# Kernel optimization log

Hardware: AMD Instinct MI355X
Metric: run time of the kernel (lower is better)

## Reference

```python
import jax, jax.numpy as jnp
import numpy as np

D_MODEL = 1024
NUM_HEADS = 16
HEAD_DIM = D_MODEL // NUM_HEADS
B, S = 4, 2048
NEG = -1e10


def setup_inputs() -> dict:
    key = jax.random.key(0)
    ks = jax.random.split(key, 10)
    s = 1.0 / np.sqrt(D_MODEL)
    x = jax.random.normal(ks[0], (B, S, D_MODEL), dtype=jnp.float32)
    mask = jnp.ones((B, S, S), dtype=jnp.int32)
    Wq = jax.random.uniform(ks[1], (D_MODEL, D_MODEL), jnp.float32, -s, s)
    bq = jnp.zeros((D_MODEL,), jnp.float32)
    Wk = jax.random.uniform(ks[2], (D_MODEL, D_MODEL), jnp.float32, -s, s)
    bk = jnp.zeros((D_MODEL,), jnp.float32)
    Wv = jax.random.uniform(ks[3], (D_MODEL, D_MODEL), jnp.float32, -s, s)
    bv = jnp.zeros((D_MODEL,), jnp.float32)
    Wo = jax.random.uniform(ks[4], (D_MODEL, D_MODEL), jnp.float32, -s, s)
    bo = jnp.zeros((D_MODEL,), jnp.float32)
    return {"x": x, "mask": mask, "Wq": Wq, "bq": bq, "Wk": Wk, "bk": bk,
            "Wv": Wv, "bv": bv, "Wo": Wo, "bo": bo}


def reference(x, mask, Wq, bq, Wk, bk, Wv, bv, Wo, bo):
    # x: [B,S,D]; projections then split into heads -> [B,H,S,hd]
    def split_heads(t):
        return t.reshape(B, S, NUM_HEADS, HEAD_DIM).transpose(0, 2, 1, 3)

    q = split_heads(x @ Wq + bq)
    k = split_heads(x @ Wk + bk)
    v = split_heads(x @ Wv + bv)
    scale = jnp.sqrt(jnp.float32(HEAD_DIM))
    # energy: [B,H,S,S]
    energy = jnp.einsum('bhqd,bhkd->bhqk', q, k) / scale
    energy = jnp.where(mask[:, None, :, :] == 0, jnp.float32(NEG), energy)
    attn = jax.nn.softmax(energy, axis=-1)
    # dropout is identity in eval mode
    out = jnp.einsum('bhqk,bhkd->bhqd', attn, v)
    out = out.transpose(0, 2, 1, 3).reshape(B, S, D_MODEL)
    return out @ Wo + bo
```

## Files before the change

### kernel.cpp

```cpp
#include <hip/hip_runtime.h>
#include <stdint.h>


#define SS 2048
#define NH 16

typedef __bf16 bf16x8 __attribute__((ext_vector_type(8)));
typedef float f32x4 __attribute__((ext_vector_type(4)));

__device__ __forceinline__ unsigned short f2bf(float f) {
  union { float f; unsigned int u; } v; v.f = f;
  unsigned int u = v.u;
  return (unsigned short)((u + 0x7fffu + ((u >> 16) & 1u)) >> 16);
}

__device__ __forceinline__ unsigned int cvtpk(float a, float b) {
  unsigned int r;
  asm("v_cvt_pk_bf16_f32 %0, %1, %2" : "=v"(r) : "v"(a), "v"(b));
  return r;
}

__device__ __forceinline__ float ex2(float x) {
  float r; asm("v_exp_f32 %0, %1" : "=v"(r) : "v"(x)); return r;
}

__device__ __forceinline__ void swap32(unsigned int& a, unsigned int& b) {
  asm volatile("v_permlane32_swap_b32 %0, %1" : "+v"(a), "+v"(b));
}
__device__ __forceinline__ void swap16(unsigned int& a, unsigned int& b) {
  asm volatile("v_permlane16_swap_b32 %0, %1" : "+v"(a), "+v"(b));
}

__device__ __forceinline__ void gload_lds16(const void* g, void* l) {
  __builtin_amdgcn_global_load_lds(
      (__attribute__((address_space(1))) void*)(void*)g,
      (__attribute__((address_space(3))) void*)l,
      16, 0, 0);
}

__global__ __launch_bounds__(256) void k_prep(const float* __restrict__ x,
                                              const float* __restrict__ W0,
                                              const float* __restrict__ W1,
                                              const float* __restrict__ W2,
                                              const float* __restrict__ W3,
                                              const int* __restrict__ mask,
                                              unsigned short* __restrict__ xb,
                                              unsigned short* __restrict__ Wt,
                                              int* __restrict__ flg) {
  __shared__ float t[64][65];
  __shared__ int s4[4];
  const int bid = blockIdx.x;
  const int tid = threadIdx.x;

  if (bid < 8192) {
    long i = ((long)bid * 256 + tid) * 4;
    float4 v = *(const float4*)(x + i);
    uint2 o;
    o.x = cvtpk(v.x, v.y);
    o.y = cvtpk(v.z, v.w);
    *(uint2*)(xb + i) = o;
  } else if (bid < 9216) {
    int inner = bid - 8192;
    int bx = inner & 15, by = (inner >> 4) & 15, bz = inner >> 8;
    const float* W = bz == 0 ? W0 : bz == 1 ? W1 : bz == 2 ? W2 : W3;
    unsigned short* dst = Wt + (size_t)bz * 1024 * 1024;
    int r0 = by * 64, c0 = bx * 64;
    int tr = tid >> 6, tc = tid & 63;
#pragma unroll
    for (int i = 0; i < 16; i++) {
      int r = tr + i * 4;
      t[r][tc] = W[(size_t)(r0 + r) * 1024 + c0 + tc];
    }
    __syncthreads();
#pragma unroll
    for (int i = 0; i < 16; i++) {
      int r = tr + i * 4;
      dst[(size_t)(c0 + r) * 1024 + r0 + tc] = f2bf(t[tc][r]);
    }
  } else {
    int inner = bid - 9216;
    int kt = inner & 31, qb = (inner >> 5) & 15, b = inner >> 9;
    const int* M = mask + ((size_t)b * SS + qb * 128) * SS + kt * 64;
    int ok = 1;
#pragma unroll
    for (int i = 0; i < 8; i++) {
      int r = (tid >> 4) + i * 16;
      int4 v = *(const int4*)(M + (size_t)r * SS + (tid & 15) * 4);
      ok &= (v.x != 0) & (v.y != 0) & (v.z != 0) & (v.w != 0);
    }
    ok = __all(ok) ? 1 : 0;
    if ((tid & 63) == 0) s4[tid >> 6] = ok;
    __syncthreads();
    if (tid == 0) flg[((size_t)b * 16 + qb) * 32 + kt] = s4[0] & s4[1] & s4[2] & s4[3];
  }
}

__global__ __launch_bounds__(256) void k_gemmQKV(const unsigned short* __restrict__ A,
                                                 const unsigned short* __restrict__ Wt,
                                                 const float* __restrict__ bq,
                                                 const float* __restrict__ bk,
                                                 const float* __restrict__ bv,
                                                 unsigned short* __restrict__ Qb,
                                                 unsigned short* __restrict__ Kb,
                                                 unsigned short* __restrict__ Vtp) {
  constexpr int K = 1024, N = 1024;
  __shared__ unsigned short lA[128 * 64];
  __shared__ unsigned short lB[128 * 64];
  const int tid = threadIdx.x;
  const int lane = tid & 63, wave = tid >> 6;
  const int wr = wave >> 1, wc = wave & 1;
  const int g = lane >> 4, c = lane & 15;

  const int mat = blockIdx.x >> 9;
  const int inner = blockIdx.x & 511;
  const int xcd = inner & 7, idx = inner >> 3;
  const int by = xcd * 8 + (idx >> 3), bx = idx & 7;
  const long brow = (long)by * 128, bcol = (long)bx * 128;

  const unsigned short* Bt = Wt + ((size_t)mat << 20);
  const float* bias = mat == 0 ? bq : (mat == 1 ? bk : bv);

  f32x4 acc[4][4] = {};

  int sr[4], sch[4];
#pragma unroll
  for (int j = 0; j < 4; j++) {
    int p = j * 4096 + tid * 16;
    int r = p >> 7;
    int sl = (p >> 4) & 7;
    sr[j] = r;
    sch[j] = (sl ^ (r & 7)) * 8;
  }
  char* lbaseA = (char*)lA + wave * 1024;
  char* lbaseB = (char*)lB + wave * 1024;

  for (int k0 = 0; k0 < K; k0 += 64) {
#pragma unroll
    for (int j = 0; j < 4; j++) {
      gload_lds16(A + (brow + sr[j]) * K + k0 + sch[j], lbaseA + j * 4096);
      gload_lds16(Bt + (bcol + sr[j]) * K + k0 + sch[j], lbaseB + j * 4096);
    }
    __syncthreads();
#pragma unroll
    for (int ks = 0; ks < 2; ks++) {
      bf16x8 af[4], bfr[4];
#pragma unroll
      for (int m = 0; m < 4; m++) {
        int ra = wr * 64 + m * 16 + c;
        af[m] = *(const bf16x8*)((const char*)lA + ra * 128 + ((ks * 64 + g * 16) ^ ((ra & 7) << 4)));
        int rb = wc * 64 + m * 16 + c;
        bfr[m] = *(const bf16x8*)((const char*)lB + rb * 128 + ((ks * 64 + g * 16) ^ ((rb & 7) << 4)));
      }
      __builtin_amdgcn_s_setprio(1);
#pragma unroll
      for (int m = 0; m < 4; m++)
#pragma unroll
        for (int n = 0; n < 4; n++)
          acc[m][n] = __builtin_amdgcn_mfma_f32_16x16x32_bf16(af[m], bfr[n], acc[m][n], 0, 0, 0);
      __builtin_amdgcn_s_setprio(0);
    }
    __syncthreads();
  }

  const float scale = (mat == 0) ? 0.180336880111120f  : 1.0f;
#pragma unroll
  for (int m = 0; m < 4; m++) {
#pragma unroll
    for (int n = 0; n < 4; n++) {
      long row0 = brow + wr * 64 + m * 16 + g * 4;
      long col = bcol + wc * 64 + n * 16 + c;
      float bv_ = bias[col];
      if (mat == 2) {
        long b_ = row0 >> 11, s = row0 & 2047;
        size_t base = ((size_t)(b_ * NH + (col >> 6)) * 64 + (col & 63)) * SS + s;
        ushort4 pk;
        pk.x = f2bf(acc[m][n][0] + bv_);
        pk.y = f2bf(acc[m][n][1] + bv_);
        pk.z = f2bf(acc[m][n][2] + bv_);
        pk.w = f2bf(acc[m][n][3] + bv_);
        *(ushort4*)(Vtp + base) = pk;
      } else {
        unsigned short* C = mat ? Kb : Qb;
#pragma unroll
        for (int r = 0; r < 4; r++)
          C[(row0 + r) * N + col] = f2bf((acc[m][n][r] + bv_) * scale);
      }
    }
  }
}

__global__ __launch_bounds__(256) void k_gemmO(const unsigned short* __restrict__ A,
                                               const unsigned short* __restrict__ Bt,
                                               const float* __restrict__ bias,
                                               float* __restrict__ Cout) {
  constexpr int K = 1024, N = 1024;
  __shared__ unsigned short lA[128 * 64];
  __shared__ unsigned short lB[128 * 64];
  const int tid = threadIdx.x;
  const int lane = tid & 63, wave = tid >> 6;
  const int wr = wave >> 1, wc = wave & 1;
  const int g = lane >> 4, c = lane & 15;

  const int bid = blockIdx.x;
  const int xcd = bid & 7, idx = bid >> 3;
  const int by = xcd * 8 + (idx >> 3), bx = idx & 7;
  const long brow = (long)by * 128, bcol = (long)bx * 128;

  f32x4 acc[4][4] = {};

  int sr[4], sch[4];
#pragma unroll
  for (int j = 0; j < 4; j++) {
    int p = j * 4096 + tid * 16;
    int r = p >> 7;
    int sl = (p >> 4) & 7;
    sr[j] = r;
    sch[j] = (sl ^ (r & 7)) * 8;
  }
  char* lbaseA = (char*)lA + wave * 1024;
  char* lbaseB = (char*)lB + wave * 1024;

  for (int k0 = 0; k0 < K; k0 += 64) {
#pragma unroll
    for (int j = 0; j < 4; j++) {
      gload_lds16(A + (brow + sr[j]) * K + k0 + sch[j], lbaseA + j * 4096);
      gload_lds16(Bt + (bcol + sr[j]) * K + k0 + sch[j], lbaseB + j * 4096);
    }
    __syncthreads();
#pragma unroll
    for (int ks = 0; ks < 2; ks++) {
      bf16x8 af[4], bfr[4];
#pragma unroll
      for (int m = 0; m < 4; m++) {
        int ra = wr * 64 + m * 16 + c;
        af[m] = *(const bf16x8*)((const char*)lA + ra * 128 + ((ks * 64 + g * 16) ^ ((ra & 7) << 4)));
        int rb = wc * 64 + m * 16 + c;
        bfr[m] = *(const bf16x8*)((const char*)lB + rb * 128 + ((ks * 64 + g * 16) ^ ((rb & 7) << 4)));
      }
      __builtin_amdgcn_s_setprio(1);
#pragma unroll
      for (int m = 0; m < 4; m++)
#pragma unroll
        for (int n = 0; n < 4; n++)
          acc[m][n] = __builtin_amdgcn_mfma_f32_16x16x32_bf16(af[m], bfr[n], acc[m][n], 0, 0, 0);
      __builtin_amdgcn_s_setprio(0);
    }
    __syncthreads();
  }

#pragma unroll
  for (int m = 0; m < 4; m++) {
#pragma unroll
    for (int n = 0; n < 4; n++) {
      long row0 = brow + wr * 64 + m * 16 + g * 4;
      long col = bcol + wc * 64 + n * 16 + c;
      float bv = bias[col];
#pragma unroll
      for (int r = 0; r < 4; r++)
        Cout[(row0 + r) * N + col] = acc[m][n][r] + bv;
    }
  }
}

__global__ __launch_bounds__(256, 4) void k_flash(const unsigned short* __restrict__ Q,
                                                  const unsigned short* __restrict__ Kb,
                                                  const unsigned short* __restrict__ Vt,
                                                  const int* __restrict__ mask,
                                                  const int* __restrict__ flg,
                                                  unsigned short* __restrict__ O) {
  __shared__ unsigned short lK[3][4096];
  __shared__ unsigned short lV[2][4096];
  const int tid = threadIdx.x, lane = tid & 63, w = tid >> 6;
  const int g = lane >> 4, c = lane & 15;

  const int bid = blockIdx.x;
  const int xcd = bid & 7, jj = bid >> 3;
  const int qb = jj & 15, Ghi = jj >> 4;
  const int G = xcd * 8 + Ghi;
  const int h = G & 15, b = G >> 4;

  const int q0 = qb * 128 + w * 32;
  const long mrow0 = (long)b * SS + q0;

  const unsigned short* Kbase = Kb + (size_t)b * SS * 1024 + h * 64;
  const unsigned short* Vbase = Vt + (size_t)((b * NH + h) * 64) * SS;
  const int* Mbase = mask + ((size_t)b * SS + q0) * SS;
  const int* Fbase = flg + ((size_t)b * 16 + qb) * 32;

  int allok = 1;
#pragma unroll
  for (int i = 0; i < 32; i++) allok &= Fbase[i];
  allok = __builtin_amdgcn_readfirstlane(allok);

  bf16x8 qf[2][2];
#pragma unroll
  for (int rt = 0; rt < 2; rt++)
#pragma unroll
    for (int ks = 0; ks < 2; ks++)
      qf[rt][ks] = *(const bf16x8*)(Q + (mrow0 + rt * 16 + c) * 1024 + h * 64 + ks * 32 + g * 8);

  const int pB = tid * 16;
  const int r0 = pB >> 7;
  const int co = (((pB >> 4) & 7) ^ (r0 & 7)) * 8;
  const unsigned short* gK = Kbase + (size_t)r0 * 1024 + co;
  const unsigned short* gV = Vbase + (size_t)r0 * SS + co;
  const int wb = w * 1024;

  char* sk0 = (char*)&lK[0][0];
  char* sk1 = (char*)&lK[1][0];
  char* sk2 = (char*)&lK[2][0];
  char* sv0 = (char*)&lV[0][0];
  char* sv1 = (char*)&lV[1][0];

#define STAGE_K(kt_, dst_) do { \
    const unsigned short* aK_ = gK + (size_t)(kt_) * (64 * 1024); \
    gload_lds16(aK_, (dst_) + wb); \
    gload_lds16(aK_ + 32 * 1024, (dst_) + wb + 4096); } while (0)
#define STAGE_V(kt_, dst_) do { \
    const unsigned short* aV_ = gV + (size_t)(kt_) * 64; \
    gload_lds16(aV_, (dst_) + wb); \
    gload_lds16(aV_ + 32 * (size_t)SS, (dst_) + wb + 4096); } while (0)

  STAGE_K(0, sk0);
  STAGE_V(0, sv0);
  STAGE_K(1, sk1);

  float mst[2] = {8.0f, 8.0f}, lst[2] = {0.0f, 0.0f};
  f32x4 o[2][4] = {};

  for (int kt = 0; kt < SS / 64; kt++) {
    if (kt < SS / 64 - 1) asm volatile("s_waitcnt vmcnt(2)" ::: "memory");
    else                  asm volatile("s_waitcnt vmcnt(0)" ::: "memory");
    __builtin_amdgcn_s_barrier();
    __builtin_amdgcn_sched_barrier(0);
    if (kt + 1 < SS / 64) STAGE_V(kt + 1, sv1);
    if (kt + 2 < SS / 64) STAGE_K(kt + 2, sk2);

    bf16x8 kf[4][2];
#pragma unroll
    for (int ct = 0; ct < 4; ct++)
#pragma unroll
      for (int ks = 0; ks < 2; ks++)
        kf[ct][ks] = *(const bf16x8*)(sk0 + (ct * 16 + c) * 128 +
                                      ((ks * 64 + g * 16) ^ ((c & 7) << 4)));

    f32x4 sc[2][4];
#pragma unroll
    for (int rt = 0; rt < 2; rt++)
#pragma unroll
      for (int ct = 0; ct < 4; ct++)
#pragma unroll
        for (int r = 0; r < 4; r++) sc[rt][ct][r] = -mst[rt];
    __builtin_amdgcn_s_setprio(1);
#pragma unroll
    for (int ks = 0; ks < 2; ks++)
#pragma unroll
      for (int rt = 0; rt < 2; rt++)
#pragma unroll
        for (int ct = 0; ct < 4; ct++)
          sc[rt][ct] = __builtin_amdgcn_mfma_f32_16x16x32_bf16(kf[ct][ks], qf[rt][ks], sc[rt][ct], 0, 0, 0);
    __builtin_amdgcn_s_setprio(0);

    if (!allok) {
      const int key0 = kt * 64;
#pragma unroll
      for (int rt = 0; rt < 2; rt++)
#pragma unroll
        for (int ct = 0; ct < 4; ct++)
#pragma unroll
          for (int r = 0; r < 4; r++) {
            int mv = Mbase[(size_t)(rt * 16 + c) * SS + key0 + ct * 16 + g * 4 + r];
            if (mv == 0) sc[rt][ct][r] = -1e10f;
          }
    }

    float pm[2];
#pragma unroll
    for (int rt = 0; rt < 2; rt++) {
      f32x4 m4;
#pragma unroll
      for (int r = 0; r < 4; r++)
        m4[r] = fmaxf(fmaxf(sc[rt][0][r], sc[rt][1][r]), fmaxf(sc[rt][2][r], sc[rt][3][r]));
      pm[rt] = fmaxf(fmaxf(m4[0], m4[1]), fmaxf(m4[2], m4[3]));
    }
    if (__any((pm[0] > 8.0f) | (pm[1] > 8.0f))) {
#pragma unroll
      for (int rt = 0; rt < 2; rt++) {
        float tmv = pm[rt];
        tmv = fmaxf(tmv, __shfl_xor(tmv, 16, 64));
        tmv = fmaxf(tmv, __shfl_xor(tmv, 32, 64));
        float dpos = fmaxf(tmv, 0.0f);
        float sf = ex2(-dpos);
        mst[rt] += dpos;
        lst[rt] *= sf;
#pragma unroll
        for (int ct = 0; ct < 4; ct++)
#pragma unroll
          for (int r = 0; r < 4; r++) { o[rt][ct][r] *= sf; sc[rt][ct][r] -= dpos; }
      }
    }

    union PU { unsigned int wd[4]; bf16x8 v; };
    PU pf[2][2];
#pragma unroll
    for (int rt = 0; rt < 2; rt++) {
      f32x4 ts4 = {0.0f, 0.0f, 0.0f, 0.0f};
      unsigned int Wd[4][2];
#pragma unroll
      for (int ct = 0; ct < 4; ct++) {
        f32x4 p;
#pragma unroll
        for (int r = 0; r < 4; r++) {
          p[r] = ex2(sc[rt][ct][r]);
          ts4[r] += p[r];
        }
        Wd[ct][0] = cvtpk(p[0], p[1]);
        Wd[ct][1] = cvtpk(p[2], p[3]);
      }
#pragma unroll
      for (int ks = 0; ks < 2; ks++)
#pragma unroll
        for (int hh = 0; hh < 2; hh++) {
          unsigned int a = Wd[2 * ks][hh], bb = Wd[2 * ks + 1][hh];
          swap32(a, bb);
          swap16(a, bb);
          pf[rt][ks].wd[hh] = a;
          pf[rt][ks].wd[2 + hh] = bb;
        }
      lst[rt] += (ts4[0] + ts4[1]) + (ts4[2] + ts4[3]);
    }

    bf16x8 vf[4][2];
#pragma unroll
    for (int ct = 0; ct < 4; ct++)
#pragma unroll
      for (int ks = 0; ks < 2; ks++)
        vf[ct][ks] = *(const bf16x8*)(sv0 + (ct * 16 + c) * 128 +
                                      ((ks * 64 + g * 16) ^ ((c & 7) << 4)));
    __builtin_amdgcn_s_setprio(1);
#pragma unroll
    for (int rt = 0; rt < 2; rt++)
#pragma unroll
      for (int ct = 0; ct < 4; ct++)
#pragma unroll
        for (int ks = 0; ks < 2; ks++)
          o[rt][ct] = __builtin_amdgcn_mfma_f32_16x16x32_bf16(vf[ct][ks], pf[rt][ks].v, o[rt][ct], 0, 0, 0);
    __builtin_amdgcn_s_setprio(0);

    char* tk = sk0; sk0 = sk1; sk1 = sk2; sk2 = tk;
    char* tv = sv0; sv0 = sv1; sv1 = tv;
  }

#pragma unroll
  for (int rt = 0; rt < 2; rt++) {
    float t = lst[rt];
    t += __shfl_xor(t, 16, 64);
    t += __shfl_xor(t, 32, 64);
    float inv = 1.0f / t;
#pragma unroll
    for (int ct = 0; ct < 4; ct++) {
      uint2 pk;
      pk.x = cvtpk(o[rt][ct][0] * inv, o[rt][ct][1] * inv);
      pk.y = cvtpk(o[rt][ct][2] * inv, o[rt][ct][3] * inv);
      *(uint2*)(O + (mrow0 + rt * 16 + c) * 1024 + h * 64 + ct * 16 + g * 4) = pk;
    }
  }
#undef STAGE_K
#undef STAGE_V
}

extern "C" void kernel_launch(void* const* d_in, const int* in_sizes, int n_in,
                              void* d_out, int out_size, void* d_ws, size_t ws_size,
                              hipStream_t stream) {
  const float* x  = (const float*)d_in[0];
  const int* mask = (const int*)d_in[1];
  const float* Wq = (const float*)d_in[2];
  const float* bq = (const float*)d_in[3];
  const float* Wk = (const float*)d_in[4];
  const float* bk = (const float*)d_in[5];
  const float* Wv = (const float*)d_in[6];
  const float* bv = (const float*)d_in[7];
  const float* Wo = (const float*)d_in[8];
  const float* bo = (const float*)d_in[9];

  char* ws = (char*)d_ws;
  unsigned short* xb = (unsigned short*)ws;
  unsigned short* Wt = (unsigned short*)(ws + (16ull << 20));
  unsigned short* Qb = (unsigned short*)(ws + (24ull << 20));
  unsigned short* Kb = (unsigned short*)(ws + (40ull << 20));
  unsigned short* Vt = (unsigned short*)(ws + (56ull << 20));
  int* flg = (int*)d_out;

  k_prep<<<11264, 256, 0, stream>>>(x, Wq, Wk, Wv, Wo, mask, xb, Wt, flg);
  k_gemmQKV<<<1536, 256, 0, stream>>>(xb, Wt, bq, bk, bv, Qb, Kb, Vt);
  k_flash<<<1024, 256, 0, stream>>>(Qb, Kb, Vt, mask, flg, xb);
  k_gemmO<<<512, 256, 0, stream>>>(xb, Wt + (3u << 20), bo, (float*)d_out);
}
```

Baseline: 200.3 us.

## Halve flash-attention tiles to 16 query rows per wave and 32-key blocks

Shrinks the attention work per wave from 32 query rows to 16, and the key/value block from 64 to 32 keys. The grid doubles to 2048 blocks and LDS buffers are halved, with a new swizzle for the narrower V tile. The aim is more concurrent blocks and lower register and LDS pressure. In exchange, each staged K/V tile is reused by half as many query rows, so global and LDS traffic per FLOP doubles, and there are twice as many loop iterations and barriers.

```diff
diff --git a/kernel.cpp b/kernel.cpp
--- a/kernel.cpp
+++ b/kernel.cpp
@@ -268,43 +268,43 @@
                                                   const int* __restrict__ mask,
                                                   const int* __restrict__ flg,
                                                   unsigned short* __restrict__ O) {
-  __shared__ unsigned short lK[3][4096];
-  __shared__ unsigned short lV[2][4096];
+  __shared__ unsigned short lK[3][2048];
+  __shared__ unsigned short lV[2][2048];
   const int tid = threadIdx.x, lane = tid & 63, w = tid >> 6;
   const int g = lane >> 4, c = lane & 15;
 
   const int bid = blockIdx.x;
   const int xcd = bid & 7, jj = bid >> 3;
-  const int qb = jj & 15, Ghi = jj >> 4;
+  const int qb = jj & 31, Ghi = jj >> 5;
   const int G = xcd * 8 + Ghi;
   const int h = G & 15, b = G >> 4;
 
-  const int q0 = qb * 128 + w * 32;
+  const int q0 = qb * 64 + w * 16;
   const long mrow0 = (long)b * SS + q0;
 
   const unsigned short* Kbase = Kb + (size_t)b * SS * 1024 + h * 64;
   const unsigned short* Vbase = Vt + (size_t)((b * NH + h) * 64) * SS;
   const int* Mbase = mask + ((size_t)b * SS + q0) * SS;
-  const int* Fbase = flg + ((size_t)b * 16 + qb) * 32;
+  const int* Fbase = flg + ((size_t)b * 16 + (q0 >> 7)) * 32;
 
   int allok = 1;
 #pragma unroll
   for (int i = 0; i < 32; i++) allok &= Fbase[i];
   allok = __builtin_amdgcn_readfirstlane(allok);
 
-  bf16x8 qf[2][2];
-#pragma unroll
-  for (int rt = 0; rt < 2; rt++)
-#pragma unroll
-    for (int ks = 0; ks < 2; ks++)
-      qf[rt][ks] = *(const bf16x8*)(Q + (mrow0 + rt * 16 + c) * 1024 + h * 64 + ks * 32 + g * 8);
+  bf16x8 qf[2];
+#pragma unroll
+  for (int ks = 0; ks < 2; ks++)
+    qf[ks] = *(const bf16x8*)(Q + (mrow0 + c) * 1024 + h * 64 + ks * 32 + g * 8);
 
   const int pB = tid * 16;
-  const int r0 = pB >> 7;
-  const int co = (((pB >> 4) & 7) ^ (r0 & 7)) * 8;
-  const unsigned short* gK = Kbase + (size_t)r0 * 1024 + co;
-  const unsigned short* gV = Vbase + (size_t)r0 * SS + co;
-  const int wb = w * 1024;
+  const int rK = pB >> 7;
+  const int coK = ((((pB >> 4) & 7) ^ (rK & 7))) * 8;
+  const unsigned short* gK = Kbase + (size_t)rK * 1024 + coK;
+  const int rV = pB >> 6;
+  const int swV = (rV & 3) ^ ((rV >> 2) & 3);
+  const int coV = (((pB >> 4) & 3) ^ swV) * 8;
+  const unsigned short* gV = Vbase + (size_t)rV * SS + coV;
 
   char* sk0 = (char*)&lK[0][0];
   char* sk1 = (char*)&lK[1][0];
@@ -312,158 +312,133 @@
   char* sv0 = (char*)&lV[0][0];
   char* sv1 = (char*)&lV[1][0];
 
-#define STAGE_K(kt_, dst_) do { \
-    const unsigned short* aK_ = gK + (size_t)(kt_) * (64 * 1024); \
-    gload_lds16(aK_, (dst_) + wb); \
-    gload_lds16(aK_ + 32 * 1024, (dst_) + wb + 4096); } while (0)
-#define STAGE_V(kt_, dst_) do { \
-    const unsigned short* aV_ = gV + (size_t)(kt_) * 64; \
-    gload_lds16(aV_, (dst_) + wb); \
-    gload_lds16(aV_ + 32 * (size_t)SS, (dst_) + wb + 4096); } while (0)
+#define STAGE_K(kt_, dst_) gload_lds16(gK + (size_t)(kt_) * (32 * 1024), (dst_) + pB)
+#define STAGE_V(kt_, dst_) gload_lds16(gV + (size_t)(kt_) * 32, (dst_) + pB)
 
   STAGE_K(0, sk0);
   STAGE_V(0, sv0);
   STAGE_K(1, sk1);
 
-  float mst[2] = {8.0f, 8.0f}, lst[2] = {0.0f, 0.0f};
-  f32x4 o[2][4] = {};
-
-  for (int kt = 0; kt < SS / 64; kt++) {
-    if (kt < SS / 64 - 1) asm volatile("s_waitcnt vmcnt(2)" ::: "memory");
-    else                  asm volatile("s_waitcnt vmcnt(0)" ::: "memory");
+  float mst = 8.0f, lst = 0.0f;
+  f32x4 o[4] = {};
+
+  constexpr int NT = SS / 32;
+  for (int kt = 0; kt < NT; kt++) {
+    if (kt < NT - 1) asm volatile("s_waitcnt vmcnt(1)" ::: "memory");
+    else             asm volatile("s_waitcnt vmcnt(0)" ::: "memory");
     __builtin_amdgcn_s_barrier();
     __builtin_amdgcn_sched_barrier(0);
-    if (kt + 1 < SS / 64) STAGE_V(kt + 1, sv1);
-    if (kt + 2 < SS / 64) STAGE_K(kt + 2, sk2);
-
-    bf16x8 kf[4][2];
-#pragma unroll
-    for (int ct = 0; ct < 4; ct++)
+    if (kt + 1 < NT) STAGE_V(kt + 1, sv1);
+    if (kt + 2 < NT) STAGE_K(kt + 2, sk2);
+
+    bf16x8 kf[2][2];
+#pragma unroll
+    for (int ct = 0; ct < 2; ct++)
 #pragma unroll
       for (int ks = 0; ks < 2; ks++)
         kf[ct][ks] = *(const bf16x8*)(sk0 + (ct * 16 + c) * 128 +
                                       ((ks * 64 + g * 16) ^ ((c & 7) << 4)));
 
-    f32x4 sc[2][4];
-#pragma unroll
-    for (int rt = 0; rt < 2; rt++)
+    f32x4 sc[2];
+#pragma unroll
+    for (int ct = 0; ct < 2; ct++)
+#pragma unroll
+      for (int r = 0; r < 4; r++) sc[ct][r] = -mst;
+    __builtin_amdgcn_s_setprio(1);
+#pragma unroll
+    for (int ks = 0; ks < 2; ks++)
+#pragma unroll
+      for (int ct = 0; ct < 2; ct++)
+        sc[ct] = __builtin_amdgcn_mfma_f32_16x16x32_bf16(kf[ct][ks], qf[ks], sc[ct], 0, 0, 0);
+    __builtin_amdgcn_s_setprio(0);
+
+    if (!allok) {
+      const int key0 = kt * 32;
+#pragma unroll
+      for (int ct = 0; ct < 2; ct++)
+#pragma unroll
+        for (int r = 0; r < 4; r++) {
+          int mv = Mbase[(size_t)c * SS + key0 + ct * 16 + g * 4 + r];
+          if (mv == 0) sc[ct][r] = -1e10f;
+        }
+    }
+
+    f32x4 m4;
+#pragma unroll
+    for (int r = 0; r < 4; r++) m4[r] = fmaxf(sc[0][r], sc[1][r]);
+    float pm = fmaxf(fmaxf(m4[0], m4[1]), fmaxf(m4[2], m4[3]));
+    if (__any(pm > 8.0f)) {
+      float tmv = pm;
+      tmv = fmaxf(tmv, __shfl_xor(tmv, 16, 64));
+      tmv = fmaxf(tmv, __shfl_xor(tmv, 32, 64));
+      float dpos = fmaxf(tmv, 0.0f);
+      float sf = ex2(-dpos);
+      mst += dpos;
+      lst *= sf;
 #pragma unroll
       for (int ct = 0; ct < 4; ct++)
 #pragma unroll
-        for (int r = 0; r < 4; r++) sc[rt][ct][r] = -mst[rt];
-    __builtin_amdgcn_s_setprio(1);
-#pragma unroll
-    for (int ks = 0; ks < 2; ks++)
-#pragma unroll
-      for (int rt = 0; rt < 2; rt++)
-#pragma unroll
-        for (int ct = 0; ct < 4; ct++)
-          sc[rt][ct] = __builtin_amdgcn_mfma_f32_16x16x32_bf16(kf[ct][ks], qf[rt][ks], sc[rt][ct], 0, 0, 0);
-    __builtin_amdgcn_s_setprio(0);
-
-    if (!allok) {
-      const int key0 = kt * 64;
-#pragma unroll
-      for (int rt = 0; rt < 2; rt++)
-#pragma unroll
-        for (int ct = 0; ct < 4; ct++)
-#pragma unroll
-          for (int r = 0; r < 4; r++) {
-            int mv = Mbase[(size_t)(rt * 16 + c) * SS + key0 + ct * 16 + g * 4 + r];
-            if (mv == 0) sc[rt][ct][r] = -1e10f;
-          }
-    }
-
-    float pm[2];
-#pragma unroll
-    for (int rt = 0; rt < 2; rt++) {
-      f32x4 m4;
-#pragma unroll
-      for (int r = 0; r < 4; r++)
-        m4[r] = fmaxf(fmaxf(sc[rt][0][r], sc[rt][1][r]), fmaxf(sc[rt][2][r], sc[rt][3][r]));
-      pm[rt] = fmaxf(fmaxf(m4[0], m4[1]), fmaxf(m4[2], m4[3]));
-    }
-    if (__any((pm[0] > 8.0f) | (pm[1] > 8.0f))) {
-#pragma unroll
-      for (int rt = 0; rt < 2; rt++) {
-        float tmv = pm[rt];
-        tmv = fmaxf(tmv, __shfl_xor(tmv, 16, 64));
-        tmv = fmaxf(tmv, __shfl_xor(tmv, 32, 64));
-        float dpos = fmaxf(tmv, 0.0f);
-        float sf = ex2(-dpos);
-        mst[rt] += dpos;
-        lst[rt] *= sf;
-#pragma unroll
-        for (int ct = 0; ct < 4; ct++)
-#pragma unroll
-          for (int r = 0; r < 4; r++) { o[rt][ct][r] *= sf; sc[rt][ct][r] -= dpos; }
-      }
+        for (int r = 0; r < 4; r++) o[ct][r] *= sf;
+#pragma unroll
+      for (int ct = 0; ct < 2; ct++)
+#pragma unroll
+        for (int r = 0; r < 4; r++) sc[ct][r] -= dpos;
     }
 
     union PU { unsigned int wd[4]; bf16x8 v; };
-    PU pf[2][2];
-#pragma unroll
-    for (int rt = 0; rt < 2; rt++) {
+    PU pf;
+    {
       f32x4 ts4 = {0.0f, 0.0f, 0.0f, 0.0f};
-      unsigned int Wd[4][2];
-#pragma unroll
-      for (int ct = 0; ct < 4; ct++) {
+      unsigned int Wd[2][2];
+#pragma unroll
+      for (int ct = 0; ct < 2; ct++) {
         f32x4 p;
 #pragma unroll
         for (int r = 0; r < 4; r++) {
-          p[r] = ex2(sc[rt][ct][r]);
+          p[r] = ex2(sc[ct][r]);
           ts4[r] += p[r];
         }
         Wd[ct][0] = cvtpk(p[0], p[1]);
         Wd[ct][1] = cvtpk(p[2], p[3]);
       }
 #pragma unroll
-      for (int ks = 0; ks < 2; ks++)
-#pragma unroll
-        for (int hh = 0; hh < 2; hh++) {
-          unsigned int a = Wd[2 * ks][hh], bb = Wd[2 * ks + 1][hh];
-          swap32(a, bb);
-          swap16(a, bb);
-          pf[rt][ks].wd[hh] = a;
-          pf[rt][ks].wd[2 + hh] = bb;
-        }
-      lst[rt] += (ts4[0] + ts4[1]) + (ts4[2] + ts4[3]);
-    }
-
-    bf16x8 vf[4][2];
+      for (int hh = 0; hh < 2; hh++) {
+        unsigned int a = Wd[0][hh], bb = Wd[1][hh];
+        swap32(a, bb);
+        swap16(a, bb);
+        pf.wd[hh] = a;
+        pf.wd[2 + hh] = bb;
+      }
+      lst += (ts4[0] + ts4[1]) + (ts4[2] + ts4[3]);
+    }
+
+    bf16x8 vf[4];
+#pragma unroll
+    for (int ct = 0; ct < 4; ct++) {
+      int row = ct * 16 + c;
+      int sw = ((row & 3) ^ ((row >> 2) & 3)) << 4;
+      vf[ct] = *(const bf16x8*)(sv0 + row * 64 + ((g * 16) ^ sw));
+    }
+    __builtin_amdgcn_s_setprio(1);
 #pragma unroll
     for (int ct = 0; ct < 4; ct++)
-#pragma unroll
-      for (int ks = 0; ks < 2; ks++)
-        vf[ct][ks] = *(const bf16x8*)(sv0 + (ct * 16 + c) * 128 +
-                                      ((ks * 64 + g * 16) ^ ((c & 7) << 4)));
-    __builtin_amdgcn_s_setprio(1);
-#pragma unroll
-    for (int rt = 0; rt < 2; rt++)
-#pragma unroll
-      for (int ct = 0; ct < 4; ct++)
-#pragma unroll
-        for (int ks = 0; ks < 2; ks++)
-          o[rt][ct] = __builtin_amdgcn_mfma_f32_16x16x32_bf16(vf[ct][ks], pf[rt][ks].v, o[rt][ct], 0, 0, 0);
+      o[ct] = __builtin_amdgcn_mfma_f32_16x16x32_bf16(vf[ct], pf.v, o[ct], 0, 0, 0);
     __builtin_amdgcn_s_setprio(0);
 
     char* tk = sk0; sk0 = sk1; sk1 = sk2; sk2 = tk;
     char* tv = sv0; sv0 = sv1; sv1 = tv;
   }
 
-#pragma unroll
-  for (int rt = 0; rt < 2; rt++) {
-    float t = lst[rt];
-    t += __shfl_xor(t, 16, 64);
-    t += __shfl_xor(t, 32, 64);
-    float inv = 1.0f / t;
-#pragma unroll
-    for (int ct = 0; ct < 4; ct++) {
-      uint2 pk;
-      pk.x = cvtpk(o[rt][ct][0] * inv, o[rt][ct][1] * inv);
-      pk.y = cvtpk(o[rt][ct][2] * inv, o[rt][ct][3] * inv);
-      *(uint2*)(O + (mrow0 + rt * 16 + c) * 1024 + h * 64 + ct * 16 + g * 4) = pk;
-    }
+  float t = lst;
+  t += __shfl_xor(t, 16, 64);
+  t += __shfl_xor(t, 32, 64);
+  float inv = 1.0f / t;
+#pragma unroll
+  for (int ct = 0; ct < 4; ct++) {
+    uint2 pk;
+    pk.x = cvtpk(o[ct][0] * inv, o[ct][1] * inv);
+    pk.y = cvtpk(o[ct][2] * inv, o[ct][3] * inv);
+    *(uint2*)(O + (mrow0 + c) * 1024 + h * 64 + ct * 16 + g * 4) = pk;
   }
 #undef STAGE_K
 #undef STAGE_V
@@ -493,6 +468,6 @@
 
   k_prep<<<11264, 256, 0, stream>>>(x, Wq, Wk, Wv, Wo, mask, xb, Wt, flg);
   k_gemmQKV<<<1536, 256, 0, stream>>>(xb, Wt, bq, bk, bv, Qb, Kb, Vt);
-  k_flash<<<1024, 256, 0, stream>>>(Qb, Kb, Vt, mask, flg, xb);
+  k_flash<<<2048, 256, 0, stream>>>(Qb, Kb, Vt, mask, flg, xb);
   k_gemmO<<<512, 256, 0, stream>>>(xb, Wt + (3u << 20), bo, (float*)d_out);
 }
```

Measured after the change: 218.9 us. 9.3% more time.
